# Kernel optimization log

Hardware: AMD Instinct MI355X
Metric: run time of the kernel (lower is better)

## Reference

```python
import jax, jax.numpy as jnp
import numpy as np

# layer dims of the hard-coded linear chain (torch Linear: y = x @ W.T + b)
_DIMS = [784, 69, 31, 10, 10, 10, 10, 10, 10, 10]


def setup_inputs() -> dict:
    key = jax.random.key(0)
    ks = jax.random.split(key, 1 + 2 * 9)
    inp = {"x": jax.random.normal(ks[0], (65536, 784), dtype=jnp.float32)}
    for i in range(9):
        fan_in, fan_out = _DIMS[i], _DIMS[i + 1]
        bound = 1.0 / np.sqrt(fan_in)
        inp[f"W{i}"] = jax.random.uniform(ks[1 + 2 * i], (fan_out, fan_in), dtype=jnp.float32, minval=-bound, maxval=bound)
        inp[f"b{i}"] = jax.random.uniform(ks[2 + 2 * i], (fan_out,), dtype=jnp.float32, minval=-bound, maxval=bound)
    return inp


def reference(x, W0, b0, W1, b1, W2, b2, W3, b3, W4, b4, W5, b5, W6, b6, W7, b7, W8, b8):
    Ws = [W0, W1, W2, W3, W4, W5, W6, W7, W8]
    bs = [b0, b1, b2, b3, b4, b5, b6, b7, b8]
    for W, b in zip(Ws, bs):
        x = x @ W.T + b  # [B, out]
    return x
```

## Files before the change

### kernel.cpp

```cpp
#include <hip/hip_runtime.h>


__global__ void prep_all(
    const float* __restrict__ W0,
    const float* __restrict__ W1, const float* __restrict__ b1,
    const float* __restrict__ W2, const float* __restrict__ b2,
    const float* __restrict__ W3, const float* __restrict__ b3,
    const float* __restrict__ W4, const float* __restrict__ b4,
    const float* __restrict__ W5, const float* __restrict__ b5,
    const float* __restrict__ W6, const float* __restrict__ b6,
    const float* __restrict__ W7, const float* __restrict__ b7,
    const float* __restrict__ W8, const float* __restrict__ b8,
    const float* __restrict__ b0,
    float* __restrict__ Wt2, float* __restrict__ beff)
{
    __shared__ float Sa[31 * 69], Sb[31 * 69];
    __shared__ float da[31], db[31];
    const int t = threadIdx.x;
    const int nt = blockDim.x;

    for (int i = t; i < 31 * 69; i += nt) Sa[i] = W1[i];
    for (int i = t; i < 31; i += nt) da[i] = b1[i];
    __syncthreads();

    for (int i = t; i < 10 * 69; i += nt) {
        int o = i / 69, c = i - o * 69;
        float s = 0.f;
        for (int k = 0; k < 31; k++) s += W2[o * 31 + k] * Sa[k * 69 + c];
        Sb[i] = s;
    }
    for (int i = t; i < 10; i += nt) {
        float s = b2[i];
        for (int k = 0; k < 31; k++) s += W2[i * 31 + k] * da[k];
        db[i] = s;
    }
    __syncthreads();

    const float* Wk[6] = { W3, W4, W5, W6, W7, W8 };
    const float* bk[6] = { b3, b4, b5, b6, b7, b8 };
    int src = 1;
    for (int st = 0; st < 6; st++) {
        const float* W = Wk[st];
        const float* bb = bk[st];
        float* S  = src ? Sb : Sa;
        float* D  = src ? Sa : Sb;
        float* dd = src ? db : da;
        float* dn = src ? da : db;
        for (int i = t; i < 10 * 69; i += nt) {
            int o = i / 69, c = i - o * 69;
            float s = 0.f;
            for (int k = 0; k < 10; k++) s += W[o * 10 + k] * S[k * 69 + c];
            D[i] = s;
        }
        for (int i = t; i < 10; i += nt) {
            float s = bb[i];
            for (int k = 0; k < 10; k++) s += W[i * 10 + k] * dd[k];
            dn[i] = s;
        }
        __syncthreads();
        src ^= 1;
    }

    float* S  = src ? Sb : Sa;
    float* dd = src ? db : da;

    if (blockIdx.x == 0) {
        for (int i = t; i < 10; i += nt) {
            float s = dd[i];
            for (int k = 0; k < 69; k++) s += S[i * 69 + k] * b0[k];
            beff[i] = s;
        }
    }

    int e = blockIdx.x * nt + t;
    if (e < 8800) {
        int j4 = e / 44, rem = e - j4 * 44;
        float val = 0.f;
        if (rem < 40) {
            int o = rem >> 2, k = rem & 3, j = j4 * 4 + k;
            if (j < 784) {
                for (int u = 0; u < 69; u++) val += S[o * 69 + u] * W0[u * 784 + j];
            }
        }
        Wt2[e] = val;
    }
}


__global__ __launch_bounds__(512, 8) void linear_main(
    const float* __restrict__ x, const float* __restrict__ Wt2,
    const float* __restrict__ beff, float* __restrict__ out)
{
    __shared__ float4 wlds[2200];
    const int t = threadIdx.x;
    const int s = t & 7;
    const long row = (long)blockIdx.x * 64 + (t >> 3);
    const float* xrow = x + row * 784;

    {
        const float4* wg = (const float4*)Wt2;
        for (int i = t; i < 2200; i += 512) wlds[i] = wg[i];
    }

    float acc[10];
#pragma unroll
    for (int o = 0; o < 10; o++) acc[o] = 0.f;

    float4 xv = *(const float4*)(xrow + s * 4);
    __syncthreads();

    for (int jb = 0; jb < 25; jb++) {
        float4 xc = xv;
        if (jb < 24) {
            int jn = (jb + 1) * 32 + s * 4;
            jn = jn > 780 ? 780 : jn;
            xv = *(const float4*)(xrow + jn);
        }
        const float4* wrow = &wlds[(jb * 8 + s) * 11];
#pragma unroll
        for (int o = 0; o < 10; o++) {
            float4 wv = wrow[o];
            acc[o] = fmaf(xc.x, wv.x, acc[o]);
            acc[o] = fmaf(xc.y, wv.y, acc[o]);
            acc[o] = fmaf(xc.z, wv.z, acc[o]);
            acc[o] = fmaf(xc.w, wv.w, acc[o]);
        }
    }

#pragma unroll
    for (int m = 1; m < 8; m <<= 1)
#pragma unroll
        for (int o = 0; o < 10; o++) acc[o] += __shfl_xor(acc[o], m, 64);

    if (s < 5) {
        float lo = 0.f, hi = 0.f;
#pragma unroll
        for (int o = 0; o < 5; o++) {
            if (s == o) { lo = acc[2 * o]; hi = acc[2 * o + 1]; }
        }
        lo += beff[s * 2];
        hi += beff[s * 2 + 1];
        *(float2*)(out + row * 10 + s * 2) = make_float2(lo, hi);
    }
}

extern "C" void kernel_launch(void* const* d_in, const int* in_sizes, int n_in,
                              void* d_out, int out_size, void* d_ws, size_t ws_size,
                              hipStream_t stream) {
    const float* x  = (const float*)d_in[0];
    const float* W0 = (const float*)d_in[1];
    const float* b0 = (const float*)d_in[2];
    const float* W1 = (const float*)d_in[3];
    const float* b1 = (const float*)d_in[4];
    const float* W2 = (const float*)d_in[5];
    const float* b2 = (const float*)d_in[6];
    const float* W3 = (const float*)d_in[7];
    const float* b3 = (const float*)d_in[8];
    const float* W4 = (const float*)d_in[9];
    const float* b4 = (const float*)d_in[10];
    const float* W5 = (const float*)d_in[11];
    const float* b5 = (const float*)d_in[12];
    const float* W6 = (const float*)d_in[13];
    const float* b6 = (const float*)d_in[14];
    const float* W7 = (const float*)d_in[15];
    const float* b7 = (const float*)d_in[16];
    const float* W8 = (const float*)d_in[17];
    const float* b8 = (const float*)d_in[18];

    float* ws   = (float*)d_ws;
    float* Wt2  = ws;
    float* beff = ws + 8800;

    float* out = (float*)d_out;
    const int B = in_sizes[0] / 784;

    prep_all<<<18, 512, 0, stream>>>(W0, W1, b1, W2, b2, W3, b3, W4, b4,
                                     W5, b5, W6, b6, W7, b7, W8, b8,
                                     b0, Wt2, beff);
    linear_main<<<B / 64, 512, 0, stream>>>(x, Wt2, beff, out);
}
```

Before: 336.7 us.

## Stream x through double-buffered LDS with coalesced loads and register prefetch

The main kernel now has each block process 256 rows in 16 chunks of 16 rows. Each chunk is loaded from global memory with fully coalesced float4 accesses into registers, then stored into a double-buffered LDS tile while the current chunk is computed. Each half-wave reduces one row across 32 lanes instead of 8 lanes per row, which removes the strided per-row global reads of the old layout. In exchange, LDS use rises to about 135KB per block, limiting residency to one 8-wave block per CU. Latency hiding then depends on the explicit register prefetch.

```diff
diff --git a/kernel.cpp b/kernel.cpp
--- a/kernel.cpp
+++ b/kernel.cpp
@@ -87,60 +87,100 @@
 }
 
 
-__global__ __launch_bounds__(512, 8) void linear_main(
+__global__ __launch_bounds__(512, 2) void linear_stream(
     const float* __restrict__ x, const float* __restrict__ Wt2,
     const float* __restrict__ beff, float* __restrict__ out)
 {
     __shared__ float4 wlds[2200];
+    __shared__ float4 xb[2][3136];
+
     const int t = threadIdx.x;
-    const int s = t & 7;
-    const long row = (long)blockIdx.x * 64 + (t >> 3);
-    const float* xrow = x + row * 784;
+    const int w = t >> 6;
+    const int r = (t >> 5) & 1;
+    const int s = t & 31;
+    const long blk_f4 = (long)blockIdx.x * 50176;
+    const float4* xg = (const float4*)x;
 
     {
         const float4* wg = (const float4*)Wt2;
         for (int i = t; i < 2200; i += 512) wlds[i] = wg[i];
     }
 
-    float acc[10];
-#pragma unroll
-    for (int o = 0; o < 10; o++) acc[o] = 0.f;
-
-    float4 xv = *(const float4*)(xrow + s * 4);
+    float beL = 0.f, beH = 0.f;
+    if (s < 5) { beL = beff[2 * s]; beH = beff[2 * s + 1]; }
+
+    float4 xgr[7];
+#pragma unroll
+    for (int k = 0; k < 6; k++) xgr[k] = xg[blk_f4 + k * 512 + t];
+    if (t < 64) xgr[6] = xg[blk_f4 + 3072 + t];
+#pragma unroll
+    for (int k = 0; k < 6; k++) xb[0][k * 512 + t] = xgr[k];
+    if (t < 64) xb[0][3072 + t] = xgr[6];
     __syncthreads();
 
-    for (int jb = 0; jb < 25; jb++) {
-        float4 xc = xv;
-        if (jb < 24) {
-            int jn = (jb + 1) * 32 + s * 4;
-            jn = jn > 780 ? 780 : jn;
-            xv = *(const float4*)(xrow + jn);
-        }
-        const float4* wrow = &wlds[(jb * 8 + s) * 11];
-#pragma unroll
-        for (int o = 0; o < 10; o++) {
-            float4 wv = wrow[o];
-            acc[o] = fmaf(xc.x, wv.x, acc[o]);
-            acc[o] = fmaf(xc.y, wv.y, acc[o]);
-            acc[o] = fmaf(xc.z, wv.z, acc[o]);
-            acc[o] = fmaf(xc.w, wv.w, acc[o]);
-        }
-    }
-
-#pragma unroll
-    for (int m = 1; m < 8; m <<= 1)
-#pragma unroll
-        for (int o = 0; o < 10; o++) acc[o] += __shfl_xor(acc[o], m, 64);
-
-    if (s < 5) {
-        float lo = 0.f, hi = 0.f;
-#pragma unroll
-        for (int o = 0; o < 5; o++) {
-            if (s == o) { lo = acc[2 * o]; hi = acc[2 * o + 1]; }
-        }
-        lo += beff[s * 2];
-        hi += beff[s * 2 + 1];
-        *(float2*)(out + row * 10 + s * 2) = make_float2(lo, hi);
+    for (int c = 0; c < 16; c++) {
+        if (c < 15) {
+            const long base = blk_f4 + (long)(c + 1) * 3136;
+#pragma unroll
+            for (int k = 0; k < 6; k++) xgr[k] = xg[base + k * 512 + t];
+            if (t < 64) xgr[6] = xg[base + 3072 + t];
+        }
+
+        const float4* xrow = &xb[c & 1][(2 * w + r) * 196];
+        float acc[10];
+#pragma unroll
+        for (int o = 0; o < 10; o++) acc[o] = 0.f;
+
+#pragma unroll
+        for (int it = 0; it < 6; it++) {
+            float4 xc = xrow[it * 32 + s];
+            const float4* wr = &wlds[(it * 32 + s) * 11];
+#pragma unroll
+            for (int o = 0; o < 10; o++) {
+                float4 wv = wr[o];
+                acc[o] = fmaf(xc.x, wv.x, acc[o]);
+                acc[o] = fmaf(xc.y, wv.y, acc[o]);
+                acc[o] = fmaf(xc.z, wv.z, acc[o]);
+                acc[o] = fmaf(xc.w, wv.w, acc[o]);
+            }
+        }
+        if (s < 4) {
+            float4 xc = xrow[192 + s];
+            const float4* wr = &wlds[(192 + s) * 11];
+#pragma unroll
+            for (int o = 0; o < 10; o++) {
+                float4 wv = wr[o];
+                acc[o] = fmaf(xc.x, wv.x, acc[o]);
+                acc[o] = fmaf(xc.y, wv.y, acc[o]);
+                acc[o] = fmaf(xc.z, wv.z, acc[o]);
+                acc[o] = fmaf(xc.w, wv.w, acc[o]);
+            }
+        }
+
+#pragma unroll
+        for (int m = 1; m < 32; m <<= 1)
+#pragma unroll
+            for (int o = 0; o < 10; o++) acc[o] += __shfl_xor(acc[o], m, 64);
+
+        {
+            const long row = (long)blockIdx.x * 256 + c * 16 + 2 * w + r;
+            if (s < 5) {
+                float lo = 0.f, hi = 0.f;
+#pragma unroll
+                for (int o = 0; o < 5; o++) {
+                    if (s == o) { lo = acc[2 * o]; hi = acc[2 * o + 1]; }
+                }
+                *(float2*)(out + row * 10 + s * 2) = make_float2(lo + beL, hi + beH);
+            }
+        }
+
+        if (c < 15) {
+            float4* dst = xb[(c + 1) & 1];
+#pragma unroll
+            for (int k = 0; k < 6; k++) dst[k * 512 + t] = xgr[k];
+            if (t < 64) dst[3072 + t] = xgr[6];
+            __syncthreads();
+        }
     }
 }
 
@@ -177,5 +217,5 @@
     prep_all<<<18, 512, 0, stream>>>(W0, W1, b1, W2, b2, W3, b3, W4, b4,
                                      W5, b5, W6, b6, W7, b7, W8, b8,
                                      b0, Wt2, beff);
-    linear_main<<<B / 64, 512, 0, stream>>>(x, Wt2, beff, out);
+    linear_stream<<<B / 256, 512, 0, stream>>>(x, Wt2, beff, out);
 }
```

Measured after the change: 364.8 us. +8.3%, slower.
